# Kernel optimization log

Hardware: AMD Instinct MI355X
Metric: run time of the kernel (lower is better)

## Reference

```python
import jax, jax.numpy as jnp
import numpy as np

C, H, P = 128, 4, 8  # d_model, n_heads, n_points (n_levels=1)
D = C // H


def setup_inputs() -> dict:
    key = jax.random.key(0)
    ks = jax.random.split(key, 14)
    B, Y, X = 2, 200, 200
    N = Y * X
    s = 0.05
    inp = {
        "query": jax.random.normal(ks[0], (B, N, C), jnp.float32),
        "query_pos": jax.random.normal(ks[1], (B, N, C), jnp.float32),
        # MSDeformAttn params
        "Wv": jax.random.normal(ks[2], (C, C), jnp.float32) * s,
        "bv": jnp.zeros((C,), jnp.float32),
        "Woff": jax.random.normal(ks[3], (C, H * P * 2), jnp.float32) * s,
        "boff": jax.random.normal(ks[4], (H * P * 2,), jnp.float32) * s,
        "Wattn": jax.random.normal(ks[5], (C, H * P), jnp.float32) * s,
        "battn": jnp.zeros((H * P,), jnp.float32),
        "Wout1": jax.random.normal(ks[6], (C, C), jnp.float32) * s,  # MSDeformAttn.output_proj
        "bout1": jnp.zeros((C,), jnp.float32),
        "Wout2": jax.random.normal(ks[7], (C, C), jnp.float32) * s,  # wrapper output_proj
        "bout2": jnp.zeros((C,), jnp.float32),
        "Y": Y,
        "X": X,
    }
    return inp


def _deform_attn(q, v_in, Wv, bv, Woff, boff, Wattn, battn, Wout1, bout1, Y, X):
    B, N, _ = q.shape
    # reference points: grid centers, stacked (y, x) normalized (as in source)
    ref_y = (jnp.arange(Y, dtype=jnp.float32) + 0.5) / Y
    ref_x = (jnp.arange(X, dtype=jnp.float32) + 0.5) / X
    ry, rx = jnp.meshgrid(ref_y, ref_x, indexing="ij")
    ref = jnp.stack([ry.reshape(-1), rx.reshape(-1)], -1)  # (N, 2)

    value = (v_in @ Wv + bv).reshape(B, Y, X, H, D).transpose(0, 3, 1, 2, 4)  # (B,H,Y,X,D)
    off = (q @ Woff + boff).reshape(B, N, H, P, 2)
    attn = jax.nn.softmax((q @ Wattn + battn).reshape(B, N, H, P), axis=-1)

    # offset normalizer = (W, H) = (X, Y); loc = ref + off/norm  (faithful to source)
    norm = jnp.array([X, Y], jnp.float32)
    loc = ref[None, :, None, None, :] + off / norm  # (B,N,H,P,2)

    # grid_sample bilinear, align_corners=False, zero padding; channel 0 = x, 1 = y
    gx = loc[..., 0] * X - 0.5
    gy = loc[..., 1] * Y - 0.5
    x0 = jnp.floor(gx)
    y0 = jnp.floor(gy)
    wx1 = gx - x0
    wy1 = gy - y0
    x0i = x0.astype(jnp.int32)
    y0i = y0.astype(jnp.int32)

    b_idx = jnp.arange(B)[:, None, None, None]
    h_idx = jnp.arange(H)[None, None, :, None]

    def gather(yi, xi, w):
        valid = (yi >= 0) & (yi < Y) & (xi >= 0) & (xi < X)
        yc = jnp.clip(yi, 0, Y - 1)
        xc = jnp.clip(xi, 0, X - 1)
        v = value[b_idx, h_idx, yc, xc]  # (B,N,H,P,D)
        return v * (w * valid)[..., None]

    sampled = (
        gather(y0i, x0i, (1 - wy1) * (1 - wx1))
        + gather(y0i, x0i + 1, (1 - wy1) * wx1)
        + gather(y0i + 1, x0i, wy1 * (1 - wx1))
        + gather(y0i + 1, x0i + 1, wy1 * wx1)
    )
    out = (sampled * attn[..., None]).sum(axis=3).reshape(B, N, C)
    return out @ Wout1 + bout1


def reference(query, query_pos, Wv, bv, Woff, boff, Wattn, battn, Wout1, bout1, Wout2, bout2, Y, X):
    residual = query
    q = query + query_pos
    out = _deform_attn(q, q, Wv, bv, Woff, boff, Wattn, battn, Wout1, bout1, Y, X)
    out = out @ Wout2 + bout2  # wrapper output_proj; dropout in eval mode = identity
    return out + residual
```

## Files before the change

### kernel.cpp

```cpp
#include <hip/hip_runtime.h>
#include <hip/hip_bf16.h>
#include <hip/hip_fp16.h>

#define BQ 2
#define YY 200
#define XX 200
#define NQ 40000
#define CC 128
#define MTOT 80000
#define NCOL 224
#define NTILES 5000

typedef __attribute__((ext_vector_type(8))) short short8;
typedef __attribute__((ext_vector_type(4))) short short4v;
typedef __attribute__((ext_vector_type(4))) float f32x4;

static __device__ __forceinline__ unsigned short f2bf(float f) {
    union { float f; unsigned int u; } v; v.f = f;
    unsigned int r = v.u + 0x7FFF + ((v.u >> 16) & 1);
    return (unsigned short)(r >> 16);
}
static __device__ __forceinline__ unsigned short f2bf_hw(float f) {
    __hip_bfloat16 h = __float2bfloat16(f);
    unsigned short s;
    __builtin_memcpy(&s, &h, 2);
    return s;
}
static __device__ __forceinline__ __half2 u2h2(unsigned int u) {
    __half2 h; __builtin_memcpy(&h, &u, 4); return h;
}
static __device__ __forceinline__ unsigned int h22u(__half2 h) {
    unsigned int u; __builtin_memcpy(&u, &h, 4); return u;
}
static __device__ __forceinline__ short h2s(__half h) {
    short s; __builtin_memcpy(&s, &h, 2); return s;
}

__global__ void prep_wcat(const float* __restrict__ Wv, const float* __restrict__ Woff,
                          const float* __restrict__ Wattn, unsigned short* __restrict__ WcatT) {
    int idx = blockIdx.x * 256 + threadIdx.x;
    if (idx >= NCOL * CC) return;
    int c = idx >> 7, k = idx & 127;
    float w = (c < 128) ? Wv[k * 128 + c]
            : (c < 192) ? Woff[k * 64 + (c - 128)]
                        : Wattn[k * 32 + (c - 192)];
    WcatT[c * 128 + k] = f2bf(w);
}

__global__ void prep_w12(const float* __restrict__ Wout1, const float* __restrict__ Wout2,
                         const float* __restrict__ bout1, const float* __restrict__ bout2,
                         unsigned short* __restrict__ W12T, float* __restrict__ b12) {
    int idx = blockIdx.x * 256 + threadIdx.x;
    int c = idx >> 7, k = idx & 127;
    float s = 0.f;
    for (int j = 0; j < 128; ++j) s += Wout1[k * 128 + j] * Wout2[j * 128 + c];
    W12T[c * 128 + k] = f2bf(s);
    if (k == 0) {
        float t = bout2[c];
        for (int j = 0; j < 128; ++j) t += bout1[j] * Wout2[j * 128 + c];
        b12[c] = t;
    }
}

__global__ __launch_bounds__(256) void qsum_kernel(const float* __restrict__ query,
                                                   const float* __restrict__ qpos,
                                                   unsigned short* __restrict__ qbf) {
    const size_t total = (size_t)MTOT * CC / 8;
    for (size_t c = (size_t)blockIdx.x * 256 + threadIdx.x; c < total;
         c += (size_t)gridDim.x * 256) {
        const float4* a = (const float4*)(query + c * 8);
        const float4* b = (const float4*)(qpos + c * 8);
        float4 a0 = a[0], a1 = a[1], b0 = b[0], b1 = b[1];
        short8 w;
        w[0] = (short)f2bf_hw(a0.x + b0.x); w[1] = (short)f2bf_hw(a0.y + b0.y);
        w[2] = (short)f2bf_hw(a0.z + b0.z); w[3] = (short)f2bf_hw(a0.w + b0.w);
        w[4] = (short)f2bf_hw(a1.x + b1.x); w[5] = (short)f2bf_hw(a1.y + b1.y);
        w[6] = (short)f2bf_hw(a1.z + b1.z); w[7] = (short)f2bf_hw(a1.w + b1.w);
        *(short8*)(qbf + c * 8) = w;
    }
}

__global__ __launch_bounds__(256, 2) void g1_kernel(
    const unsigned short* __restrict__ qbf, const unsigned short* __restrict__ WcatT,
    const float* __restrict__ bv, const float* __restrict__ boff, const float* __restrict__ battn,
    unsigned short* __restrict__ value_h, float* __restrict__ off_out, float* __restrict__ logits_out)
{
    const int tid = threadIdx.x;
    const int group = blockIdx.x >> 8;
    const int gblk = blockIdx.x & 255;
    const int lane = tid & 63;
    const int arow = lane & 15, kq = lane >> 4;
    const int wid = gblk * 4 + (tid >> 6);
    const int tg0 = group * 4;
    const int NT = (group == 3) ? 2 : 4;

    short8 bf[4][4];
#pragma unroll
    for (int t = 0; t < 4; ++t) {
        if (t < NT) {
#pragma unroll
            for (int ks = 0; ks < 4; ++ks)
                bf[t][ks] = *(const short8*)(WcatT + (size_t)((tg0 + t) * 16 + arow) * 128 + ks * 32 + kq * 8);
        }
    }

    f32x4 biasv[4];
#pragma unroll
    for (int t = 0; t < 4; ++t) {
        if (t < NT) {
            const float* bp = (group < 2) ? (bv + (tg0 + t) * 16 + kq * 4)
                            : (group == 2) ? (boff + (tg0 + t - 8) * 16 + kq * 4)
                                           : (battn + (tg0 + t - 12) * 16 + kq * 4);
            float4 b4 = *(const float4*)bp;
            biasv[t] = (f32x4){b4.x, b4.y, b4.z, b4.w};
        }
    }

    for (int tile = wid; tile < NTILES; tile += 1024) {
        const char* pa = (const char*)qbf + (size_t)(tile * 16 + arow) * 256 + kq * 16;
        short8 af[4];
#pragma unroll
        for (int ks = 0; ks < 4; ++ks) af[ks] = *(const short8*)(pa + ks * 64);

        f32x4 acc[4];
#pragma unroll
        for (int t = 0; t < 4; ++t) acc[t] = biasv[t];

#pragma unroll
        for (int ks = 0; ks < 4; ++ks) {
#pragma unroll
            for (int t = 0; t < 4; ++t) {
                if (t < NT)
                    acc[t] = __builtin_amdgcn_mfma_f32_16x16x32_bf16(bf[t][ks], af[ks], acc[t], 0, 0, 0);
            }
        }

        const int row = tile * 16 + arow;
        if (group < 2) {
#pragma unroll
            for (int t = 0; t < 4; ++t) {
                short4v pv;
                pv[0] = h2s(__float2half(acc[t][0])); pv[1] = h2s(__float2half(acc[t][1]));
                pv[2] = h2s(__float2half(acc[t][2])); pv[3] = h2s(__float2half(acc[t][3]));
                *(short4v*)(value_h + (size_t)row * 128 + (tg0 + t) * 16 + kq * 4) = pv;
            }
        } else if (group == 2) {
#pragma unroll
            for (int t = 0; t < 4; ++t) {
                float4 o = make_float4(acc[t][0], acc[t][1], acc[t][2], acc[t][3]);
                *(float4*)(off_out + (size_t)row * 64 + (tg0 + t - 8) * 16 + kq * 4) = o;
            }
        } else {
#pragma unroll
            for (int t = 0; t < 2; ++t) {
                float4 o = make_float4(acc[t][0], acc[t][1], acc[t][2], acc[t][3]);
                *(float4*)(logits_out + (size_t)row * 32 + (tg0 + t - 12) * 16 + kq * 4) = o;
            }
        }
    }
}

__global__ __launch_bounds__(256) void sample_kernel(
    const unsigned short* __restrict__ value_h, const float* __restrict__ off_in,
    const float* __restrict__ logits, unsigned short* __restrict__ sampled)
{
    __shared__ int4 SA[8][36];
    __shared__ int4 SW[8][36];

    const int tid = threadIdx.x;
    const int qi = tid >> 5;
    const int lane = tid & 31;
    const int r = blockIdx.x * 8 + qi;
    const int b = (r >= NQ) ? 1 : 0;
    const int n = r - b * NQ;
    const int yq = n / XX, xq = n - yq * XX;

    {
        float lg = logits[(size_t)r * 32 + lane];
        float m = lg;
        m = fmaxf(m, __shfl_xor(m, 1));
        m = fmaxf(m, __shfl_xor(m, 2));
        m = fmaxf(m, __shfl_xor(m, 4));
        float e = __expf(lg - m);
        float s = e;
        s += __shfl_xor(s, 1);
        s += __shfl_xor(s, 2);
        s += __shfl_xor(s, 4);
        float aw = e / s;

        float2 o = ((const float2*)(off_in + (size_t)r * 64))[lane];
        float gx = (float)yq + o.x;
        float gy = (float)xq + o.y;
        float fx = floorf(gx), fy = floorf(gy);
        int x0 = (int)fx, y0 = (int)fy;
        float wx1 = gx - fx, wy1 = gy - fy;
        float vx0 = ((unsigned)x0 < XX) ? 1.f : 0.f;
        float vx1 = ((unsigned)(x0 + 1) < XX) ? 1.f : 0.f;
        float vy0 = ((unsigned)y0 < YY) ? 1.f : 0.f;
        float vy1 = ((unsigned)(y0 + 1) < YY) ? 1.f : 0.f;
        int x0c = min(max(x0, 0), XX - 1);
        int x1c = min(max(x0 + 1, 0), XX - 1);
        int y0c = min(max(y0, 0), YY - 1);
        int y1c = min(max(y0 + 1, 0), YY - 1);
        int hb = (lane >> 3) * 64;
        int rowA = y0c * XX, rowB = y1c * XX;
        int4 addrs;
        addrs.x = (rowA + x0c) * 256 + hb;
        addrs.y = (rowA + x1c) * 256 + hb;
        addrs.z = (rowB + x0c) * 256 + hb;
        addrs.w = (rowB + x1c) * 256 + hb;

        float wxa = (1.f - wx1) * vx0;
        float wxb = wx1 * vx1;
        float wya = aw * (1.f - wy1) * vy0;
        float wyb = aw * wy1 * vy1;
        int4 wts;
        wts.x = (int)h22u(__float2half2_rn(wxa * wya));
        wts.y = (int)h22u(__float2half2_rn(wxb * wya));
        wts.z = (int)h22u(__float2half2_rn(wxa * wyb));
        wts.w = (int)h22u(__float2half2_rn(wxb * wyb));

        const int slot = (lane & 7) * 4 + (lane >> 3);
        SA[qi][slot] = addrs;
        SW[qi][slot] = wts;
    }
    __syncthreads();

    const char* vb = (const char*)(value_h + (size_t)b * NQ * 128);
    const int h = lane >> 3, yc = (lane >> 2) & 1, quad = lane & 3;
    const int cb = quad * 16;

    int2 a[8];
#pragma unroll
    for (int p = 0; p < 8; ++p)
        a[p] = *(const int2*)((const char*)&SA[qi][p * 4 + h] + yc * 8);

    uint4 d0[8], d1[8];
#pragma unroll
    for (int p = 0; p < 8; ++p) {
        d0[p] = *(const uint4*)(vb + a[p].x + cb);
        d1[p] = *(const uint4*)(vb + a[p].y + cb);
    }

    int2 w[8];
#pragma unroll
    for (int p = 0; p < 8; ++p)
        w[p] = *(const int2*)((const char*)&SW[qi][p * 4 + h] + yc * 8);

    __half2 acc0 = __float2half2_rn(0.f), acc1 = __float2half2_rn(0.f);
    __half2 acc2 = __float2half2_rn(0.f), acc3 = __float2half2_rn(0.f);

#pragma unroll
    for (int p = 0; p < 8; ++p) {
        __half2 wa = u2h2((unsigned int)w[p].x);
        __half2 wb = u2h2((unsigned int)w[p].y);
        acc0 = __hfma2(wa, u2h2(d0[p].x), acc0);
        acc1 = __hfma2(wa, u2h2(d0[p].y), acc1);
        acc2 = __hfma2(wa, u2h2(d0[p].z), acc2);
        acc3 = __hfma2(wa, u2h2(d0[p].w), acc3);
        acc0 = __hfma2(wb, u2h2(d1[p].x), acc0);
        acc1 = __hfma2(wb, u2h2(d1[p].y), acc1);
        acc2 = __hfma2(wb, u2h2(d1[p].z), acc2);
        acc3 = __hfma2(wb, u2h2(d1[p].w), acc3);
    }

    acc0 = __hadd2(acc0, u2h2((unsigned int)__shfl_xor((int)h22u(acc0), 4)));
    acc1 = __hadd2(acc1, u2h2((unsigned int)__shfl_xor((int)h22u(acc1), 4)));
    acc2 = __hadd2(acc2, u2h2((unsigned int)__shfl_xor((int)h22u(acc2), 4)));
    acc3 = __hadd2(acc3, u2h2((unsigned int)__shfl_xor((int)h22u(acc3), 4)));

    __half2 pa = (yc == 0) ? acc0 : acc2;
    __half2 pb = (yc == 0) ? acc1 : acc3;
    uint2 packed;
    packed.x = ((unsigned int)f2bf(__high2float(pa)) << 16) | (unsigned int)f2bf(__low2float(pa));
    packed.y = ((unsigned int)f2bf(__high2float(pb)) << 16) | (unsigned int)f2bf(__low2float(pb));
    *(uint2*)((char*)(sampled + (size_t)r * 128) + h * 64 + cb + yc * 8) = packed;
}

__global__ __launch_bounds__(256, 2) void g2_kernel(
    const unsigned short* __restrict__ sampled, const unsigned short* __restrict__ W12T,
    const float* __restrict__ b12, const float* __restrict__ query, float* __restrict__ out)
{
    const int tid = threadIdx.x;
    const int group = blockIdx.x >> 9;
    const int gblk = blockIdx.x & 511;
    const int lane = tid & 63;
    const int arow = lane & 15, kq = lane >> 4;
    const int wid = gblk * 4 + (tid >> 6);
    const int tg0 = group * 4;

    short8 bf[4][4];
#pragma unroll
    for (int t = 0; t < 4; ++t)
#pragma unroll
        for (int ks = 0; ks < 4; ++ks)
            bf[t][ks] = *(const short8*)(W12T + (size_t)((tg0 + t) * 16 + arow) * 128 + ks * 32 + kq * 8);

    f32x4 biasv[4];
#pragma unroll
    for (int t = 0; t < 4; ++t) {
        float4 b4 = *(const float4*)(b12 + (tg0 + t) * 16 + kq * 4);
        biasv[t] = (f32x4){b4.x, b4.y, b4.z, b4.w};
    }

    for (int tile = wid; tile < NTILES; tile += 2048) {
        const char* pa = (const char*)sampled + (size_t)(tile * 16 + arow) * 256 + kq * 16;
        short8 af[4];
#pragma unroll
        for (int ks = 0; ks < 4; ++ks) af[ks] = *(const short8*)(pa + ks * 64);

        f32x4 acc[4];
#pragma unroll
        for (int t = 0; t < 4; ++t) acc[t] = biasv[t];

#pragma unroll
        for (int ks = 0; ks < 4; ++ks)
#pragma unroll
            for (int t = 0; t < 4; ++t)
                acc[t] = __builtin_amdgcn_mfma_f32_16x16x32_bf16(bf[t][ks], af[ks], acc[t], 0, 0, 0);

        const int row = tile * 16 + arow;
#pragma unroll
        for (int t = 0; t < 4; ++t) {
            size_t idx = (size_t)row * 128 + (tg0 + t) * 16 + kq * 4;
            float4 q4 = *(const float4*)(query + idx);
            float4 o = make_float4(acc[t][0] + q4.x, acc[t][1] + q4.y,
                                   acc[t][2] + q4.z, acc[t][3] + q4.w);
            *(float4*)(out + idx) = o;
        }
    }
}

extern "C" void kernel_launch(void* const* d_in, const int* in_sizes, int n_in,
                              void* d_out, int out_size, void* d_ws, size_t ws_size,
                              hipStream_t stream) {
    const float* query = (const float*)d_in[0];
    const float* qpos  = (const float*)d_in[1];
    const float* Wv    = (const float*)d_in[2];
    const float* bv    = (const float*)d_in[3];
    const float* Woff  = (const float*)d_in[4];
    const float* boff  = (const float*)d_in[5];
    const float* Wattn = (const float*)d_in[6];
    const float* battn = (const float*)d_in[7];
    const float* Wout1 = (const float*)d_in[8];
    const float* bout1 = (const float*)d_in[9];
    const float* Wout2 = (const float*)d_in[10];
    const float* bout2 = (const float*)d_in[11];
    float* out = (float*)d_out;

    char* ws = (char*)d_ws;
    unsigned short* value_h  = (unsigned short*)(ws);
    float*          off_buf  = (float*)(ws + 20480000);
    float*          logits   = (float*)(ws + 40960000);
    unsigned short* sampled  = (unsigned short*)(ws + 51200000);
    unsigned short* WcatT    = (unsigned short*)(ws + 71680000);
    unsigned short* W12T     = (unsigned short*)(ws + 71680000 + 57344);
    float*          b12      = (float*)(ws + 71680000 + 57344 + 32768);

    unsigned short* qbf = sampled;

    prep_wcat<<<112, 256, 0, stream>>>(Wv, Woff, Wattn, WcatT);
    prep_w12<<<64, 256, 0, stream>>>(Wout1, Wout2, bout1, bout2, W12T, b12);
    qsum_kernel<<<2048, 256, 0, stream>>>(query, qpos, qbf);
    g1_kernel<<<1024, 256, 0, stream>>>(qbf, WcatT, bv, boff, battn,
                                        value_h, off_buf, logits);
    sample_kernel<<<MTOT / 8, 256, 0, stream>>>(value_h, off_buf, logits, sampled);
    g2_kernel<<<1024, 256, 0, stream>>>(sampled, W12T, b12, query, out);
}
```

Measured before the change: 113.0 us.

## Fuse query+pos sum into projection GEMM and store offsets/logits as fp16

Removes the separate qsum kernel. The GEMM kernel now loads query and query_pos in fp32, adds them and converts to bf16 in registers before the MFMA, so the intermediate bf16 buffer is never written or re-read. Offsets and attention logits are now stored as fp16 instead of fp32, which halves that intermediate traffic into the sampling kernel. The trade-offs are that each of the four column-group blocks rereads the fp32 inputs (twice the bytes of the old bf16 copy), and fp16 offsets lose precision for sampling locations.

```diff
diff --git a/kernel.cpp b/kernel.cpp
--- a/kernel.cpp
+++ b/kernel.cpp
@@ -34,6 +34,9 @@
 }
 static __device__ __forceinline__ short h2s(__half h) {
     short s; __builtin_memcpy(&s, &h, 2); return s;
+}
+static __device__ __forceinline__ unsigned int packh2(float a, float b) {
+    return h22u(__floats2half2_rn(a, b));
 }
 
 __global__ void prep_wcat(const float* __restrict__ Wv, const float* __restrict__ Woff,
@@ -62,28 +65,12 @@
     }
 }
 
-__global__ __launch_bounds__(256) void qsum_kernel(const float* __restrict__ query,
-                                                   const float* __restrict__ qpos,
-                                                   unsigned short* __restrict__ qbf) {
-    const size_t total = (size_t)MTOT * CC / 8;
-    for (size_t c = (size_t)blockIdx.x * 256 + threadIdx.x; c < total;
-         c += (size_t)gridDim.x * 256) {
-        const float4* a = (const float4*)(query + c * 8);
-        const float4* b = (const float4*)(qpos + c * 8);
-        float4 a0 = a[0], a1 = a[1], b0 = b[0], b1 = b[1];
-        short8 w;
-        w[0] = (short)f2bf_hw(a0.x + b0.x); w[1] = (short)f2bf_hw(a0.y + b0.y);
-        w[2] = (short)f2bf_hw(a0.z + b0.z); w[3] = (short)f2bf_hw(a0.w + b0.w);
-        w[4] = (short)f2bf_hw(a1.x + b1.x); w[5] = (short)f2bf_hw(a1.y + b1.y);
-        w[6] = (short)f2bf_hw(a1.z + b1.z); w[7] = (short)f2bf_hw(a1.w + b1.w);
-        *(short8*)(qbf + c * 8) = w;
-    }
-}
-
 __global__ __launch_bounds__(256, 2) void g1_kernel(
-    const unsigned short* __restrict__ qbf, const unsigned short* __restrict__ WcatT,
+    const float* __restrict__ query, const float* __restrict__ qpos,
+    const unsigned short* __restrict__ WcatT,
     const float* __restrict__ bv, const float* __restrict__ boff, const float* __restrict__ battn,
-    unsigned short* __restrict__ value_h, float* __restrict__ off_out, float* __restrict__ logits_out)
+    unsigned short* __restrict__ value_h, unsigned short* __restrict__ off_h,
+    unsigned short* __restrict__ logits_h)
 {
     const int tid = threadIdx.x;
     const int group = blockIdx.x >> 8;
@@ -117,10 +104,8 @@
     }
 
     for (int tile = wid; tile < NTILES; tile += 1024) {
-        const char* pa = (const char*)qbf + (size_t)(tile * 16 + arow) * 256 + kq * 16;
-        short8 af[4];
-#pragma unroll
-        for (int ks = 0; ks < 4; ++ks) af[ks] = *(const short8*)(pa + ks * 64);
+        const float4* pq = (const float4*)(query + (size_t)(tile * 16 + arow) * 128 + kq * 8);
+        const float4* pp = (const float4*)(qpos  + (size_t)(tile * 16 + arow) * 128 + kq * 8);
 
         f32x4 acc[4];
 #pragma unroll
@@ -128,10 +113,17 @@
 
 #pragma unroll
         for (int ks = 0; ks < 4; ++ks) {
+            float4 a0 = pq[8 * ks], a1 = pq[8 * ks + 1];
+            float4 b0 = pp[8 * ks], b1 = pp[8 * ks + 1];
+            short8 af;
+            af[0] = (short)f2bf_hw(a0.x + b0.x); af[1] = (short)f2bf_hw(a0.y + b0.y);
+            af[2] = (short)f2bf_hw(a0.z + b0.z); af[3] = (short)f2bf_hw(a0.w + b0.w);
+            af[4] = (short)f2bf_hw(a1.x + b1.x); af[5] = (short)f2bf_hw(a1.y + b1.y);
+            af[6] = (short)f2bf_hw(a1.z + b1.z); af[7] = (short)f2bf_hw(a1.w + b1.w);
 #pragma unroll
             for (int t = 0; t < 4; ++t) {
                 if (t < NT)
-                    acc[t] = __builtin_amdgcn_mfma_f32_16x16x32_bf16(bf[t][ks], af[ks], acc[t], 0, 0, 0);
+                    acc[t] = __builtin_amdgcn_mfma_f32_16x16x32_bf16(bf[t][ks], af, acc[t], 0, 0, 0);
             }
         }
 
@@ -147,22 +139,26 @@
         } else if (group == 2) {
 #pragma unroll
             for (int t = 0; t < 4; ++t) {
-                float4 o = make_float4(acc[t][0], acc[t][1], acc[t][2], acc[t][3]);
-                *(float4*)(off_out + (size_t)row * 64 + (tg0 + t - 8) * 16 + kq * 4) = o;
+                uint2 pk;
+                pk.x = packh2(acc[t][0], acc[t][1]);
+                pk.y = packh2(acc[t][2], acc[t][3]);
+                *(uint2*)(off_h + (size_t)row * 64 + (tg0 + t - 8) * 16 + kq * 4) = pk;
             }
         } else {
 #pragma unroll
             for (int t = 0; t < 2; ++t) {
-                float4 o = make_float4(acc[t][0], acc[t][1], acc[t][2], acc[t][3]);
-                *(float4*)(logits_out + (size_t)row * 32 + (tg0 + t - 12) * 16 + kq * 4) = o;
+                uint2 pk;
+                pk.x = packh2(acc[t][0], acc[t][1]);
+                pk.y = packh2(acc[t][2], acc[t][3]);
+                *(uint2*)(logits_h + (size_t)row * 32 + (tg0 + t - 12) * 16 + kq * 4) = pk;
             }
         }
     }
 }
 
 __global__ __launch_bounds__(256) void sample_kernel(
-    const unsigned short* __restrict__ value_h, const float* __restrict__ off_in,
-    const float* __restrict__ logits, unsigned short* __restrict__ sampled)
+    const unsigned short* __restrict__ value_h, const unsigned short* __restrict__ off_h,
+    const unsigned short* __restrict__ logits_h, unsigned short* __restrict__ sampled)
 {
     __shared__ int4 SA[8][36];
     __shared__ int4 SW[8][36];
@@ -176,7 +172,7 @@
     const int yq = n / XX, xq = n - yq * XX;
 
     {
-        float lg = logits[(size_t)r * 32 + lane];
+        float lg = __half2float(*(const __half*)(logits_h + (size_t)r * 32 + lane));
         float m = lg;
         m = fmaxf(m, __shfl_xor(m, 1));
         m = fmaxf(m, __shfl_xor(m, 2));
@@ -188,9 +184,9 @@
         s += __shfl_xor(s, 4);
         float aw = e / s;
 
-        float2 o = ((const float2*)(off_in + (size_t)r * 64))[lane];
-        float gx = (float)yq + o.x;
-        float gy = (float)xq + o.y;
+        __half2 oh = u2h2(*(const unsigned int*)(off_h + (size_t)r * 64 + lane * 2));
+        float gx = (float)yq + __low2float(oh);
+        float gy = (float)xq + __high2float(oh);
         float fx = floorf(gx), fy = floorf(gy);
         int x0 = (int)fx, y0 = (int)fy;
         float wx1 = gx - fx, wy1 = gy - fy;
@@ -350,20 +346,17 @@
 
     char* ws = (char*)d_ws;
     unsigned short* value_h  = (unsigned short*)(ws);
-    float*          off_buf  = (float*)(ws + 20480000);
-    float*          logits   = (float*)(ws + 40960000);
+    unsigned short* off_h    = (unsigned short*)(ws + 20480000);
+    unsigned short* logits_h = (unsigned short*)(ws + 40960000);
     unsigned short* sampled  = (unsigned short*)(ws + 51200000);
     unsigned short* WcatT    = (unsigned short*)(ws + 71680000);
     unsigned short* W12T     = (unsigned short*)(ws + 71680000 + 57344);
     float*          b12      = (float*)(ws + 71680000 + 57344 + 32768);
 
-    unsigned short* qbf = sampled;
-
     prep_wcat<<<112, 256, 0, stream>>>(Wv, Woff, Wattn, WcatT);
     prep_w12<<<64, 256, 0, stream>>>(Wout1, Wout2, bout1, bout2, W12T, b12);
-    qsum_kernel<<<2048, 256, 0, stream>>>(query, qpos, qbf);
-    g1_kernel<<<1024, 256, 0, stream>>>(qbf, WcatT, bv, boff, battn,
-                                        value_h, off_buf, logits);
-    sample_kernel<<<MTOT / 8, 256, 0, stream>>>(value_h, off_buf, logits, sampled);
+    g1_kernel<<<1024, 256, 0, stream>>>(query, qpos, WcatT, bv, boff, battn,
+                                        value_h, off_h, logits_h);
+    sample_kernel<<<MTOT / 8, 256, 0, stream>>>(value_h, off_h, logits_h, sampled);
     g2_kernel<<<1024, 256, 0, stream>>>(sampled, W12T, b12, query, out);
 }
```

Result: slower. 133.6 us (+18.2%).
